# Performance work log

Hardware: AMD Instinct MI355X
Metric: run time of the kernel (lower is better)

Reference implementation:

```python
import jax, jax.numpy as jnp
import numpy as np
import math

B, T, D, H = 2, 2048, 1024, 16
HD = D // H
EPS = 1e-5


def layer_norm(x, gamma, beta):
    mu = jnp.mean(x, axis=-1, keepdims=True)
    var = jnp.mean(jnp.square(x - mu), axis=-1, keepdims=True)
    return (x - mu) * jax.lax.rsqrt(var + EPS) * gamma + beta


def setup_inputs() -> dict:
    key = jax.random.key(0)
    ks = jax.random.split(key, 12)
    s = 0.02
    return {
        "x": jax.random.normal(ks[0], (B, T, D), dtype=jnp.float32),
        # weights stored [in, out] (apply as x @ W)
        "w_qkv": jax.random.normal(ks[1], (D, 3 * D), dtype=jnp.float32) * s,
        "w_out": jax.random.normal(ks[2], (D, D), dtype=jnp.float32) * s,
        "w_ff1": jax.random.normal(ks[3], (D, 4 * D), dtype=jnp.float32) * s,
        "b_ff1": jnp.zeros((4 * D,), dtype=jnp.float32),
        "w_ff2": jax.random.normal(ks[4], (4 * D, D), dtype=jnp.float32) * s,
        "b_ff2": jnp.zeros((D,), dtype=jnp.float32),
        "g1": jnp.ones((D,), dtype=jnp.float32),
        "be1": jnp.zeros((D,), dtype=jnp.float32),
        "g2": jnp.ones((D,), dtype=jnp.float32),
        "be2": jnp.zeros((D,), dtype=jnp.float32),
    }


def reference(x, w_qkv, w_out, w_ff1, b_ff1, w_ff2, b_ff2, g1, be1, g2, be2):
    residual = x
    xn = layer_norm(x, g1, be1)
    qkv = (xn @ w_qkv).reshape(B, T, 3, H, HD)
    q, k, v = jnp.moveaxis(qkv, 2, 0)          # each [B, T, H, HD]
    scale = 1.0 / math.sqrt(HD)
    attn = jnp.einsum("bqhd,bkhd->bhqk", q, k) * scale  # [B,H,T,T]
    attn = jax.nn.softmax(attn, axis=-1)
    out = jnp.einsum("bhqk,bkhd->bqhd", attn, v).reshape(B, T, D)
    out = out @ w_out
    x = residual + out
    residual = x
    xn = layer_norm(x, g2, be2)
    h = jax.nn.gelu(xn @ w_ff1 + b_ff1, approximate=False)  # torch nn.GELU = exact erf
    x = residual + (h @ w_ff2 + b_ff2)
    return x
```

## Files before the change

### kernel.cpp

```cpp
#include <hip/hip_runtime.h>
#include <math.h>

#define Bc 2
#define Tc 2048
#define Dc 1024
#define Hc 16
#define HDc 64
#define Mc (Bc * Tc)

typedef __attribute__((ext_vector_type(4))) float f32x4;
typedef __attribute__((ext_vector_type(8))) short bf16x8;

__device__ __forceinline__ unsigned short f2bf(float f) {
  unsigned int u = __float_as_uint(f);
  u += 0x7fff + ((u >> 16) & 1);
  return (unsigned short)(u >> 16);
}

__device__ __forceinline__ void gload16(const void* g, void* l) {
  __builtin_amdgcn_global_load_lds((const __attribute__((address_space(1))) unsigned int*)g,
                                   (__attribute__((address_space(3))) unsigned int*)l, 16, 0, 0);
}

__global__ __launch_bounds__(256) void wconv_all(const float* __restrict__ w0, const float* __restrict__ w1,
                                                 const float* __restrict__ w2, const float* __restrict__ w3,
                                                 unsigned short* __restrict__ o0, unsigned short* __restrict__ o1,
                                                 unsigned short* __restrict__ o2, unsigned short* __restrict__ o3) {
  __shared__ float tile[64][65];
  int bid = blockIdx.x;
  const float* W; unsigned short* Wt; int K, N, tx;
  if (bid < 768)       { W = w0; Wt = o0; K = 1024; N = 3072; tx = 48; }
  else if (bid < 1024) { bid -= 768;  W = w1; Wt = o1; K = 1024; N = 1024; tx = 16; }
  else if (bid < 2048) { bid -= 1024; W = w2; Wt = o2; K = 1024; N = 4096; tx = 64; }
  else                 { bid -= 2048; W = w3; Wt = o3; K = 4096; N = 1024; tx = 16; }
  const int kt = (bid / tx) * 64, nt = (bid % tx) * 64;
  const int t = threadIdx.x;
#pragma unroll
  for (int p = 0; p < 4; p++) {
    int kr = p * 16 + (t >> 4);
    int nc = (t & 15) * 4;
    float4 v = *(const float4*)&W[(size_t)(kt + kr) * N + nt + nc];
    tile[kr][nc] = v.x; tile[kr][nc + 1] = v.y; tile[kr][nc + 2] = v.z; tile[kr][nc + 3] = v.w;
  }
  __syncthreads();
  const int nr = t >> 2, kc = (t & 3) * 16;
  unsigned int u[8];
#pragma unroll
  for (int i = 0; i < 8; i++)
    u[i] = (unsigned int)f2bf(tile[kc + 2 * i][nr]) | ((unsigned int)f2bf(tile[kc + 2 * i + 1][nr]) << 16);
  uint4 q0; q0.x = u[0]; q0.y = u[1]; q0.z = u[2]; q0.w = u[3];
  uint4 q1; q1.x = u[4]; q1.y = u[5]; q1.z = u[6]; q1.w = u[7];
  *(uint4*)&Wt[(size_t)(nt + nr) * K + kt + kc] = q0;
  *(uint4*)&Wt[(size_t)(nt + nr) * K + kt + kc + 8] = q1;
}

__global__ __launch_bounds__(256) void ln_kernel(const float* __restrict__ x,
                                                 const float* __restrict__ g,
                                                 const float* __restrict__ be,
                                                 unsigned short* __restrict__ out) {
  const int row = blockIdx.x;
  const int t = threadIdx.x;
  const float4* xp = (const float4*)(x + (size_t)row * Dc);
  float4 v = xp[t];
  float s = v.x + v.y + v.z + v.w;
  float s2 = v.x * v.x + v.y * v.y + v.z * v.z + v.w * v.w;
#pragma unroll
  for (int off = 32; off; off >>= 1) {
    s += __shfl_down(s, off);
    s2 += __shfl_down(s2, off);
  }
  __shared__ float rs[4], rs2[4];
  if ((t & 63) == 0) { rs[t >> 6] = s; rs2[t >> 6] = s2; }
  __syncthreads();
  float S = rs[0] + rs[1] + rs[2] + rs[3];
  float S2 = rs2[0] + rs2[1] + rs2[2] + rs2[3];
  float mean = S * (1.0f / Dc);
  float var = S2 * (1.0f / Dc) - mean * mean;
  float rstd = rsqrtf(var + 1e-5f);
  float4 gv = ((const float4*)g)[t];
  float4 bv = ((const float4*)be)[t];
  float o0 = (v.x - mean) * rstd * gv.x + bv.x;
  float o1 = (v.y - mean) * rstd * gv.y + bv.y;
  float o2 = (v.z - mean) * rstd * gv.z + bv.z;
  float o3 = (v.w - mean) * rstd * gv.w + bv.w;
  uint2 pk;
  pk.x = (unsigned int)f2bf(o0) | ((unsigned int)f2bf(o1) << 16);
  pk.y = (unsigned int)f2bf(o2) | ((unsigned int)f2bf(o3) << 16);
  *(uint2*)(out + (size_t)row * Dc + t * 4) = pk;
}

template<int BM>
__global__ __launch_bounds__(256) void gemm_bf16(const unsigned short* __restrict__ A,
                                                 const unsigned short* __restrict__ Wt,
                                                 const float* __restrict__ bias,
                                                 const float* __restrict__ resid,
                                                 float* __restrict__ C,
                                                 unsigned short* __restrict__ aux,
                                                 int M, int N, int K, int flags) {
  constexpr int BN = 128;
  constexpr int NW = (BM == 128) ? 2 : 4;
  constexpr int WN = BN / NW;
  constexpr int NFR = WN / 16;
  constexpr int ALOADS = BM / 64;
  __shared__ alignas(16) unsigned short As[2][BM][32];
  __shared__ alignas(16) unsigned short Bs[2][BN][32];
  const int t = threadIdx.x;
  const int lane = t & 63, wave = t >> 6;
  const int wr = (BM == 128) ? (wave >> 1) : 0;
  const int wc = (BM == 128) ? (wave & 1) : wave;
  const int c = lane & 15, g = lane >> 4;

  const int gx = N / BN;
  const int sw = gx >> 3;
  const int bid = blockIdx.x;
  const int xcd = bid & 7, lid = bid >> 3;
  const int lx = xcd * sw + lid % sw;
  const int ly = lid / sw;
  const int row0 = ly * BM, col0 = lx * BN;

  f32x4 acc[4][NFR];
#pragma unroll
  for (int m = 0; m < 4; m++)
#pragma unroll
    for (int n = 0; n < NFR; n++) acc[m][n] = (f32x4){0.f, 0.f, 0.f, 0.f};

  auto stage = [&](int k0, int buf) {
    char* AsB = (char*)&As[buf][0][0] + wave * 1024;
    char* BsB = (char*)&Bs[buf][0][0] + wave * 1024;
#pragma unroll
    for (int i = 0; i < ALOADS; i++) {
      int l = t + 256 * i;
      gload16(A + (size_t)(row0 + (l >> 2)) * K + k0 + (l & 3) * 8, AsB + i * 4096);
    }
#pragma unroll
    for (int i = 0; i < 2; i++) {
      int l = t + 256 * i;
      gload16(Wt + (size_t)(col0 + (l >> 2)) * K + k0 + (l & 3) * 8, BsB + i * 4096);
    }
  };

  const int nk = K / 32;
  stage(0, 0);
  for (int ki = 0; ki < nk; ki++) {
    const int buf = ki & 1;
    __syncthreads();
    if (ki + 1 < nk) stage((ki + 1) * 32, buf ^ 1);
    const char* Ab = (const char*)&As[buf][0][0];
    const char* Bb = (const char*)&Bs[buf][0][0];
    bf16x8 af[4], bfv[NFR];
#pragma unroll
    for (int m = 0; m < 4; m++) af[m] = *(const bf16x8*)(Ab + (wr * 64 + m * 16 + c) * 64 + g * 16);
#pragma unroll
    for (int n = 0; n < NFR; n++) bfv[n] = *(const bf16x8*)(Bb + (wc * WN + n * 16 + c) * 64 + g * 16);
#pragma unroll
    for (int m = 0; m < 4; m++)
#pragma unroll
      for (int n = 0; n < NFR; n++)
        acc[m][n] = __builtin_amdgcn_mfma_f32_16x16x32_bf16(af[m], bfv[n], acc[m][n], 0, 0, 0);
  }

#pragma unroll
  for (int m = 0; m < 4; m++) {
    const int row = row0 + wr * 64 + m * 16 + g * 4;
#pragma unroll
    for (int n = 0; n < NFR; n++) {
      const int col = col0 + wc * WN + n * 16 + c;
      const float bi = (flags & 1) ? bias[col] : 0.0f;
#pragma unroll
      for (int r = 0; r < 4; r++) {
        float v = acc[m][n][r] + bi;
        if (flags & 2) v = 0.5f * v * (1.0f + erff(v * 0.70710678118654752f));
        if (flags & 4) v += resid[(size_t)(row + r) * N + col];
        if (flags & 16) {
          int rr = row + r;
          int b = rr >> 11, tt = rr & 2047;
          int s = col >> 10, wcol = col & 1023;
          int h = wcol >> 6, f = wcol & 63;
          size_t base = ((size_t)(b * Hc + h)) * 131072;
          unsigned short bv = f2bf(v);
          if (s == 0) {
            aux[base + (size_t)tt * HDc + f] = bv;
          } else if (s == 1) {
            aux[4194304 + base + (size_t)(tt >> 4) * 1024 + (f >> 3) * 128 + (tt & 15) * 8 + (f & 7)] = bv;
          } else {
            int kk = tt & 63;
            aux[8388608 + base + (size_t)(tt >> 6) * 4096 + (f >> 4) * 1024 +
                ((kk >> 5) & 1) * 512 + ((kk >> 3) & 3) * 128 + (f & 15) * 8 + (kk & 7)] = bv;
          }
        } else if (flags & 8) {
          aux[(size_t)(row + r) * N + col] = f2bf(v);
        } else {
          C[(size_t)(row + r) * N + col] = v;
        }
      }
    }
  }
}

__global__ __launch_bounds__(256, 4) void fattn(const unsigned short* __restrict__ Qb,
                                                const unsigned short* __restrict__ KF,
                                                const unsigned short* __restrict__ VF,
                                                unsigned short* __restrict__ Ob) {
  __shared__ alignas(16) unsigned short P[4][16][64];
  const int t = threadIdx.x, wave = t >> 6, lane = t & 63;
  const int c = lane & 15, g = lane >> 4;
  const int bid = blockIdx.x;
  const int bh = ((bid & 7) << 2) | ((bid >> 3) & 3);
  const int qt = bid >> 5;
  const int q0 = qt * 64 + wave * 16;

  const unsigned short* Qp = Qb + ((size_t)bh * Tc + q0) * HDc;
  const unsigned short* Kp = KF + (size_t)bh * 131072;
  const unsigned short* Vp = VF + (size_t)bh * 131072;
  char* Pw = (char*)&P[wave][0][0];

  const bf16x8 qf0 = *(const bf16x8*)(Qp + c * HDc + g * 8);
  const bf16x8 qf1 = *(const bf16x8*)(Qp + c * HDc + 32 + g * 8);

  const f32x4 z = {0.f, 0.f, 0.f, 0.f};
  f32x4 o[4] = {z, z, z, z};
  float m[4] = {-3e38f, -3e38f, -3e38f, -3e38f};
  float l[4] = {0.f, 0.f, 0.f, 0.f};
  float minm = -3e38f;
  const float Cs = 0.125f * 1.4426950408889634f;
  const int xc = ((c & 7) << 4) ^ ((c & 8) << 2);
  const int lofs = lane * 8;

  auto loadK = [&](int kt, bf16x8 (&K)[4][2]) {
    const unsigned short* kb = Kp + (kt >> 4) * 1024 + lofs;
#pragma unroll
    for (int i = 0; i < 4; i++) {
      K[i][0] = *(const bf16x8*)(kb + i * 1024);
      K[i][1] = *(const bf16x8*)(kb + i * 1024 + 512);
    }
  };

  auto tile = [&](int kt, bf16x8 (&K)[4][2]) {
    f32x4 s[4];
#pragma unroll
    for (int i = 0; i < 4; i++) {
      s[i] = __builtin_amdgcn_mfma_f32_16x16x32_bf16(qf0, K[i][0], z, 0, 0, 0);
      s[i] = __builtin_amdgcn_mfma_f32_16x16x32_bf16(qf1, K[i][1], s[i], 0, 0, 0);
    }
    const unsigned short* vb = Vp + (kt >> 6) * 4096 + lofs;
    bf16x8 v0[4], v1[4];
#pragma unroll
    for (int d4 = 0; d4 < 4; d4++) {
      v0[d4] = *(const bf16x8*)(vb + d4 * 1024);
      v1[d4] = *(const bf16x8*)(vb + d4 * 1024 + 512);
    }
#pragma unroll
    for (int i = 0; i < 4; i++)
#pragma unroll
      for (int r = 0; r < 4; r++) s[i][r] *= Cs;

    float LM = s[0][0];
#pragma unroll
    for (int i = 0; i < 4; i++)
#pragma unroll
      for (int r = 0; r < 4; r++) LM = fmaxf(LM, s[i][r]);

    if (!__all(LM <= minm + 8.0f)) {
#pragma unroll
      for (int r = 0; r < 4; r++) {
        float rm = fmaxf(fmaxf(s[0][r], s[1][r]), fmaxf(s[2][r], s[3][r]));
        rm = fmaxf(rm, __shfl_xor(rm, 1));
        rm = fmaxf(rm, __shfl_xor(rm, 2));
        rm = fmaxf(rm, __shfl_xor(rm, 4));
        rm = fmaxf(rm, __shfl_xor(rm, 8));
        float nm = fmaxf(m[r], rm);
        float ef = exp2f(m[r] - nm);
        m[r] = nm;
        l[r] *= ef;
        o[0][r] *= ef; o[1][r] *= ef; o[2][r] *= ef; o[3][r] *= ef;
      }
      minm = fminf(fminf(m[0], m[1]), fminf(m[2], m[3]));
    }

#pragma unroll
    for (int r = 0; r < 4; r++) {
      const int rw = g * 4 + r;
      const int xr = ((rw & 7) << 4) ^ ((rw & 8) << 2);
      float p0 = exp2f(s[0][r] - m[r]);
      float p1 = exp2f(s[1][r] - m[r]);
      float p2 = exp2f(s[2][r] - m[r]);
      float p3 = exp2f(s[3][r] - m[r]);
      l[r] += (p0 + p1) + (p2 + p3);
      *(unsigned short*)(Pw + rw * 128 + ((c * 2) ^ xr))      = f2bf(p0);
      *(unsigned short*)(Pw + rw * 128 + ((32 + c * 2) ^ xr)) = f2bf(p1);
      *(unsigned short*)(Pw + rw * 128 + ((64 + c * 2) ^ xr)) = f2bf(p2);
      *(unsigned short*)(Pw + rw * 128 + ((96 + c * 2) ^ xr)) = f2bf(p3);
    }

    const bf16x8 pf0 = *(const bf16x8*)(Pw + c * 128 + ((g * 16) ^ xc));
    const bf16x8 pf1 = *(const bf16x8*)(Pw + c * 128 + ((64 + g * 16) ^ xc));
#pragma unroll
    for (int d4 = 0; d4 < 4; d4++) {
      o[d4] = __builtin_amdgcn_mfma_f32_16x16x32_bf16(pf0, v0[d4], o[d4], 0, 0, 0);
      o[d4] = __builtin_amdgcn_mfma_f32_16x16x32_bf16(pf1, v1[d4], o[d4], 0, 0, 0);
    }
  };

  bf16x8 kA[4][2], kB[4][2];
  loadK(0, kA);
  for (int kt = 0; kt < Tc; kt += 128) {
    loadK(kt + 64, kB);
    tile(kt, kA);
    loadK((kt + 128) & (Tc - 1), kA);
    tile(kt + 64, kB);
  }

  float linv[4];
#pragma unroll
  for (int r = 0; r < 4; r++) {
    float L = l[r];
    L += __shfl_xor(L, 1); L += __shfl_xor(L, 2); L += __shfl_xor(L, 4); L += __shfl_xor(L, 8);
    linv[r] = 1.0f / L;
  }
  const int b = bh >> 4, h = bh & 15;
#pragma unroll
  for (int r = 0; r < 4; r++) {
    size_t rowoff = ((size_t)b * Tc + q0 + g * 4 + r) * Dc + h * HDc + c;
    Ob[rowoff + 0]  = f2bf(o[0][r] * linv[r]);
    Ob[rowoff + 16] = f2bf(o[1][r] * linv[r]);
    Ob[rowoff + 32] = f2bf(o[2][r] * linv[r]);
    Ob[rowoff + 48] = f2bf(o[3][r] * linv[r]);
  }
}

extern "C" void kernel_launch(void* const* d_in, const int* in_sizes, int n_in,
                              void* d_out, int out_size, void* d_ws, size_t ws_size,
                              hipStream_t stream) {
  const float* x     = (const float*)d_in[0];
  const float* w_qkv = (const float*)d_in[1];
  const float* w_out = (const float*)d_in[2];
  const float* w_ff1 = (const float*)d_in[3];
  const float* b_ff1 = (const float*)d_in[4];
  const float* w_ff2 = (const float*)d_in[5];
  const float* b_ff2 = (const float*)d_in[6];
  const float* g1    = (const float*)d_in[7];
  const float* be1   = (const float*)d_in[8];
  const float* g2    = (const float*)d_in[9];
  const float* be2   = (const float*)d_in[10];

  char* ws = (char*)d_ws;
  unsigned short* qkvb  = (unsigned short*)ws;
  unsigned short* xn    = (unsigned short*)(ws + ((size_t)24 << 20));
  unsigned short* Ob    = (unsigned short*)(ws + ((size_t)32 << 20));
  unsigned short* hbuf  = (unsigned short*)(ws + ((size_t)40 << 20));
  unsigned short* wqkvT = (unsigned short*)(ws + ((size_t)72 << 20));
  unsigned short* woutT = (unsigned short*)(ws + ((size_t)78 << 20));
  unsigned short* wff1T = (unsigned short*)(ws + ((size_t)80 << 20));
  unsigned short* wff2T = (unsigned short*)(ws + ((size_t)88 << 20));
  float* x2 = (float*)d_out;

  dim3 blk(256);
  wconv_all<<<3072, blk, 0, stream>>>(w_qkv, w_out, w_ff1, w_ff2, wqkvT, woutT, wff1T, wff2T);

  ln_kernel<<<Mc, blk, 0, stream>>>(x, g1, be1, xn);
  gemm_bf16<128><<<768, blk, 0, stream>>>(xn, wqkvT, nullptr, nullptr, nullptr, qkvb,
                                          Mc, 3 * Dc, Dc, 16);
  fattn<<<dim3(1024), blk, 0, stream>>>(qkvb, qkvb + 4194304, qkvb + 8388608, Ob);
  gemm_bf16<64><<<512, blk, 0, stream>>>(Ob, woutT, nullptr, x, x2, nullptr,
                                         Mc, Dc, Dc, 4);
  ln_kernel<<<Mc, blk, 0, stream>>>(x2, g2, be2, xn);
  gemm_bf16<128><<<1024, blk, 0, stream>>>(xn, wff1T, b_ff1, nullptr, nullptr, hbuf,
                                           Mc, 4 * Dc, Dc, 1 | 2 | 8);
  gemm_bf16<64><<<512, blk, 0, stream>>>(hbuf, wff2T, b_ff2, x2, (float*)d_out, nullptr,
                                         Mc, Dc, 4 * Dc, 1 | 4);
}
```

Before: 457.4 us.

## Compute transposed S in attention to keep P in registers, dropping LDS round-trip

The QK^T MFMA now swaps its operands, so each lane holds scores for a single query column. Softmax probabilities are packed straight into bf16 MFMA operand registers with v_cvt_pk_bf16_f32 instead of being staged through shared memory. The V layout written by the QKV GEMM epilogue is permuted to match the new P register ordering. Row max and sum now use one value per lane with cross-group shuffles and a folded scale FMA, which removes the LDS writes, reads and per-row reductions but relies on the layout permutation being exactly right.

```diff
diff --git a/kernel.cpp b/kernel.cpp
--- a/kernel.cpp
+++ b/kernel.cpp
@@ -15,6 +15,12 @@
   unsigned int u = __float_as_uint(f);
   u += 0x7fff + ((u >> 16) & 1);
   return (unsigned short)(u >> 16);
+}
+
+__device__ __forceinline__ unsigned int cvtpk(float lo, float hi) {
+  unsigned int r;
+  asm("v_cvt_pk_bf16_f32 %0, %1, %2" : "=v"(r) : "v"(lo), "v"(hi));
+  return r;
 }
 
 __device__ __forceinline__ void gload16(const void* g, void* l) {
@@ -183,9 +189,10 @@
           } else if (s == 1) {
             aux[4194304 + base + (size_t)(tt >> 4) * 1024 + (f >> 3) * 128 + (tt & 15) * 8 + (f & 7)] = bv;
           } else {
-            int kk = tt & 63;
+            int a = tt & 63;
+            int j = (((a >> 4) & 1) << 2) | (a & 3);
             aux[8388608 + base + (size_t)(tt >> 6) * 4096 + (f >> 4) * 1024 +
-                ((kk >> 5) & 1) * 512 + ((kk >> 3) & 3) * 128 + (f & 15) * 8 + (kk & 7)] = bv;
+                ((a >> 5) & 1) * 512 + ((a >> 2) & 3) * 128 + (f & 15) * 8 + j] = bv;
           }
         } else if (flags & 8) {
           aux[(size_t)(row + r) * N + col] = f2bf(v);
@@ -201,7 +208,6 @@
                                                 const unsigned short* __restrict__ KF,
                                                 const unsigned short* __restrict__ VF,
                                                 unsigned short* __restrict__ Ob) {
-  __shared__ alignas(16) unsigned short P[4][16][64];
   const int t = threadIdx.x, wave = t >> 6, lane = t & 63;
   const int c = lane & 15, g = lane >> 4;
   const int bid = blockIdx.x;
@@ -212,18 +218,15 @@
   const unsigned short* Qp = Qb + ((size_t)bh * Tc + q0) * HDc;
   const unsigned short* Kp = KF + (size_t)bh * 131072;
   const unsigned short* Vp = VF + (size_t)bh * 131072;
-  char* Pw = (char*)&P[wave][0][0];
 
   const bf16x8 qf0 = *(const bf16x8*)(Qp + c * HDc + g * 8);
   const bf16x8 qf1 = *(const bf16x8*)(Qp + c * HDc + 32 + g * 8);
 
   const f32x4 z = {0.f, 0.f, 0.f, 0.f};
   f32x4 o[4] = {z, z, z, z};
-  float m[4] = {-3e38f, -3e38f, -3e38f, -3e38f};
-  float l[4] = {0.f, 0.f, 0.f, 0.f};
-  float minm = -3e38f;
+  float m = -3e38f;
+  float l = 0.f;
   const float Cs = 0.125f * 1.4426950408889634f;
-  const int xc = ((c & 7) << 4) ^ ((c & 8) << 2);
   const int lofs = lane * 8;
 
   auto loadK = [&](int kt, bf16x8 (&K)[4][2]) {
@@ -239,8 +242,8 @@
     f32x4 s[4];
 #pragma unroll
     for (int i = 0; i < 4; i++) {
-      s[i] = __builtin_amdgcn_mfma_f32_16x16x32_bf16(qf0, K[i][0], z, 0, 0, 0);
-      s[i] = __builtin_amdgcn_mfma_f32_16x16x32_bf16(qf1, K[i][1], s[i], 0, 0, 0);
+      s[i] = __builtin_amdgcn_mfma_f32_16x16x32_bf16(K[i][0], qf0, z, 0, 0, 0);
+      s[i] = __builtin_amdgcn_mfma_f32_16x16x32_bf16(K[i][1], qf1, s[i], 0, 0, 0);
     }
     const unsigned short* vb = Vp + (kt >> 6) * 4096 + lofs;
     bf16x8 v0[4], v1[4];
@@ -249,55 +252,48 @@
       v0[d4] = *(const bf16x8*)(vb + d4 * 1024);
       v1[d4] = *(const bf16x8*)(vb + d4 * 1024 + 512);
     }
-#pragma unroll
-    for (int i = 0; i < 4; i++)
-#pragma unroll
-      for (int r = 0; r < 4; r++) s[i][r] *= Cs;
-
-    float LM = s[0][0];
-#pragma unroll
-    for (int i = 0; i < 4; i++)
-#pragma unroll
-      for (int r = 0; r < 4; r++) LM = fmaxf(LM, s[i][r]);
-
-    if (!__all(LM <= minm + 8.0f)) {
+
+    float lm = fmaxf(fmaxf(s[0][0], s[0][1]), fmaxf(s[0][2], s[0][3]));
+#pragma unroll
+    for (int i = 1; i < 4; i++)
+      lm = fmaxf(lm, fmaxf(fmaxf(s[i][0], s[i][1]), fmaxf(s[i][2], s[i][3])));
+    const float lms = lm * Cs;
+
+    if (!__all(lms <= m + 8.0f)) {
+      float mx = fmaxf(lms, __shfl_xor(lms, 16));
+      mx = fmaxf(mx, __shfl_xor(mx, 32));
+      float nm = fmaxf(m, mx);
+      float ef = exp2f(m - nm);
+      m = nm;
+      l *= ef;
 #pragma unroll
       for (int r = 0; r < 4; r++) {
-        float rm = fmaxf(fmaxf(s[0][r], s[1][r]), fmaxf(s[2][r], s[3][r]));
-        rm = fmaxf(rm, __shfl_xor(rm, 1));
-        rm = fmaxf(rm, __shfl_xor(rm, 2));
-        rm = fmaxf(rm, __shfl_xor(rm, 4));
-        rm = fmaxf(rm, __shfl_xor(rm, 8));
-        float nm = fmaxf(m[r], rm);
-        float ef = exp2f(m[r] - nm);
-        m[r] = nm;
-        l[r] *= ef;
-        o[0][r] *= ef; o[1][r] *= ef; o[2][r] *= ef; o[3][r] *= ef;
+        float efr = __shfl(ef, g * 4 + r);
+        o[0][r] *= efr; o[1][r] *= efr; o[2][r] *= efr; o[3][r] *= efr;
       }
-      minm = fminf(fminf(m[0], m[1]), fminf(m[2], m[3]));
-    }
-
-#pragma unroll
-    for (int r = 0; r < 4; r++) {
-      const int rw = g * 4 + r;
-      const int xr = ((rw & 7) << 4) ^ ((rw & 8) << 2);
-      float p0 = exp2f(s[0][r] - m[r]);
-      float p1 = exp2f(s[1][r] - m[r]);
-      float p2 = exp2f(s[2][r] - m[r]);
-      float p3 = exp2f(s[3][r] - m[r]);
-      l[r] += (p0 + p1) + (p2 + p3);
-      *(unsigned short*)(Pw + rw * 128 + ((c * 2) ^ xr))      = f2bf(p0);
-      *(unsigned short*)(Pw + rw * 128 + ((32 + c * 2) ^ xr)) = f2bf(p1);
-      *(unsigned short*)(Pw + rw * 128 + ((64 + c * 2) ^ xr)) = f2bf(p2);
-      *(unsigned short*)(Pw + rw * 128 + ((96 + c * 2) ^ xr)) = f2bf(p3);
-    }
-
-    const bf16x8 pf0 = *(const bf16x8*)(Pw + c * 128 + ((g * 16) ^ xc));
-    const bf16x8 pf1 = *(const bf16x8*)(Pw + c * 128 + ((64 + g * 16) ^ xc));
+    }
+
+    float psum = 0.f;
+#pragma unroll
+    for (int i = 0; i < 4; i++) {
+#pragma unroll
+      for (int r = 0; r < 4; r++) {
+        s[i][r] = exp2f(fmaf(s[i][r], Cs, -m));
+        psum += s[i][r];
+      }
+    }
+    l += psum;
+
+    union { unsigned int w[4]; bf16x8 v; } pk0, pk1;
+    pk0.w[0] = cvtpk(s[0][0], s[0][1]); pk0.w[1] = cvtpk(s[0][2], s[0][3]);
+    pk0.w[2] = cvtpk(s[1][0], s[1][1]); pk0.w[3] = cvtpk(s[1][2], s[1][3]);
+    pk1.w[0] = cvtpk(s[2][0], s[2][1]); pk1.w[1] = cvtpk(s[2][2], s[2][3]);
+    pk1.w[2] = cvtpk(s[3][0], s[3][1]); pk1.w[3] = cvtpk(s[3][2], s[3][3]);
+
 #pragma unroll
     for (int d4 = 0; d4 < 4; d4++) {
-      o[d4] = __builtin_amdgcn_mfma_f32_16x16x32_bf16(pf0, v0[d4], o[d4], 0, 0, 0);
-      o[d4] = __builtin_amdgcn_mfma_f32_16x16x32_bf16(pf1, v1[d4], o[d4], 0, 0, 0);
+      o[d4] = __builtin_amdgcn_mfma_f32_16x16x32_bf16(pk0.v, v0[d4], o[d4], 0, 0, 0);
+      o[d4] = __builtin_amdgcn_mfma_f32_16x16x32_bf16(pk1.v, v1[d4], o[d4], 0, 0, 0);
     }
   };
 
@@ -310,21 +306,21 @@
     tile(kt + 64, kB);
   }
 
-  float linv[4];
-#pragma unroll
-  for (int r = 0; r < 4; r++) {
-    float L = l[r];
-    L += __shfl_xor(L, 1); L += __shfl_xor(L, 2); L += __shfl_xor(L, 4); L += __shfl_xor(L, 8);
-    linv[r] = 1.0f / L;
-  }
+  l += __shfl_xor(l, 16);
+  l += __shfl_xor(l, 32);
+  const float linv = 1.0f / l;
+  float linvr[4];
+#pragma unroll
+  for (int r = 0; r < 4; r++) linvr[r] = __shfl(linv, g * 4 + r);
+
   const int b = bh >> 4, h = bh & 15;
 #pragma unroll
   for (int r = 0; r < 4; r++) {
     size_t rowoff = ((size_t)b * Tc + q0 + g * 4 + r) * Dc + h * HDc + c;
-    Ob[rowoff + 0]  = f2bf(o[0][r] * linv[r]);
-    Ob[rowoff + 16] = f2bf(o[1][r] * linv[r]);
-    Ob[rowoff + 32] = f2bf(o[2][r] * linv[r]);
-    Ob[rowoff + 48] = f2bf(o[3][r] * linv[r]);
+    Ob[rowoff + 0]  = f2bf(o[0][r] * linvr[r]);
+    Ob[rowoff + 16] = f2bf(o[1][r] * linvr[r]);
+    Ob[rowoff + 32] = f2bf(o[2][r] * linvr[r]);
+    Ob[rowoff + 48] = f2bf(o[3][r] * linvr[r]);
   }
 }
 
```

After: 435.9 us. -4.7%, faster.
